# Performance work log

Hardware: AMD Instinct MI355X
Metric: run time of the kernel (lower is better)

The kernel has to match this reference:

```python
import jax, jax.numpy as jnp
import numpy as np

B, L, D = 2, 1024, 1024
H = 16
NL = 2
DFF = 4 * D
EPS = 1e-5
W_SCALE = 0.02


def rmsnorm(x, w):
    # x * rsqrt(mean(x^2, -1) + eps) * w   (computed in fp32 as in the torch code)
    xf = x.astype(jnp.float32)
    n = xf * jax.lax.rsqrt(jnp.mean(xf * xf, axis=-1, keepdims=True) + EPS)
    return n.astype(x.dtype) * w


def setup_inputs() -> dict:
    key = jax.random.key(0)
    ks = jax.random.split(key, 10)
    x = jax.random.normal(ks[0], (B, L, D), dtype=jnp.float32)
    # torch nn.Linear weight layout: [out_features, in_features]; y = x @ W.T + b
    qw = jax.random.normal(ks[1], (NL, D, D), dtype=jnp.float32) * W_SCALE
    kw = jax.random.normal(ks[2], (NL, D, D), dtype=jnp.float32) * W_SCALE
    vw = jax.random.normal(ks[3], (NL, D, D), dtype=jnp.float32) * W_SCALE
    ow = jax.random.normal(ks[4], (NL, D, D), dtype=jnp.float32) * W_SCALE
    pn_w = jnp.ones((NL, D), dtype=jnp.float32)
    ln_w = jnp.ones((NL, D), dtype=jnp.float32)
    fc_w = jax.random.normal(ks[5], (NL, DFF, D), dtype=jnp.float32) * W_SCALE
    fc2_w = jax.random.normal(ks[6], (NL, D, DFF), dtype=jnp.float32) * W_SCALE
    fc2_b = jnp.zeros((NL, D), dtype=jnp.float32)
    return {"x": x, "qw": qw, "kw": kw, "vw": vw, "ow": ow,
            "pn_w": pn_w, "ln_w": ln_w, "fc_w": fc_w, "fc2_w": fc2_w, "fc2_b": fc2_b}


def reference(x, qw, kw, vw, ow, pn_w, ln_w, fc_w, fc2_w, fc2_b):
    d = D // H
    for i in range(NL):
        # --- LinearAttention block (dropout=0 -> identity) ---
        h = rmsnorm(x, pn_w[i])                                   # [B,L,D]
        Q = (h @ qw[i].T).reshape(B, L, H, d)
        K = (h @ kw[i].T).reshape(B, L, H, d)
        V = (h @ vw[i].T).reshape(B, L, H, d)
        # outer-product state per position, cumulated over L (causal linear attn)
        W = jnp.einsum('blhd,blhe->blhde', K, V)                  # [B,L,H,d,d]
        W = jnp.cumsum(W, axis=1)
        a = jnp.einsum('blhd,blhde->blhe', Q, W).reshape(B, L, D)
        x = x + a @ ow[i].T
        # --- MLP block ---
        m = rmsnorm(x, ln_w[i])
        f = jax.nn.gelu(m @ fc_w[i].T, approximate=False)         # torch nn.GELU default = exact
        x = x + f @ fc2_w[i].T + fc2_b[i]
    return x
```

## Files before the change

kernel.cpp:

```cpp
#include <hip/hip_runtime.h>

#define BB 2
#define LL 1024
#define DD 1024
#define HH 16
#define HD 64
#define DFFN 4096
#define MM (BB*LL)
#define QS 3072

using u16 = unsigned short;
typedef __bf16 bf16x8 __attribute__((ext_vector_type(8)));
typedef float f32x4 __attribute__((ext_vector_type(4)));

__device__ __forceinline__ float b2f(u16 u) {
  union { unsigned int i; float f; } v; v.i = ((unsigned int)u) << 16; return v.f;
}
__device__ __forceinline__ u16 f2b(float f) {
  union { float f; unsigned int i; } v; v.f = f;
  unsigned int x = v.i;
  return (u16)((x + 0x7fffu + ((x >> 16) & 1u)) >> 16);
}
__device__ __forceinline__ float gelu_exact(float x) {
  return 0.5f * x * (1.0f + erff(x * 0.70710678118654752f));
}
__device__ __forceinline__ void gl2lds16(const void* g, void* l) {
  __builtin_amdgcn_global_load_lds((const __attribute__((address_space(1))) void*)g,
                                   (__attribute__((address_space(3))) void*)l, 16, 0, 0);
}

template<int N>
__device__ __forceinline__ void s_wait_vm() {
  if constexpr (N == 0)      asm volatile("s_waitcnt vmcnt(0) lgkmcnt(0)" ::: "memory");
  else if constexpr (N == 4) asm volatile("s_waitcnt vmcnt(4) lgkmcnt(0)" ::: "memory");
  else if constexpr (N == 6) asm volatile("s_waitcnt vmcnt(6) lgkmcnt(0)" ::: "memory");
  else if constexpr (N == 8) asm volatile("s_waitcnt vmcnt(8) lgkmcnt(0)" ::: "memory");
  __builtin_amdgcn_sched_barrier(0);
}

__global__ __launch_bounds__(256) void castw_kernel(const float* __restrict__ in,
                                                    u16* __restrict__ out, int n8) {
  int i = blockIdx.x * 256 + threadIdx.x;
  if (i >= n8) return;
  const float4 a = reinterpret_cast<const float4*>(in)[2 * i];
  const float4 b = reinterpret_cast<const float4*>(in)[2 * i + 1];
  uint4 o;
  o.x = (unsigned)f2b(a.x) | ((unsigned)f2b(a.y) << 16);
  o.y = (unsigned)f2b(a.z) | ((unsigned)f2b(a.w) << 16);
  o.z = (unsigned)f2b(b.x) | ((unsigned)f2b(b.y) << 16);
  o.w = (unsigned)f2b(b.z) | ((unsigned)f2b(b.w) << 16);
  reinterpret_cast<uint4*>(out)[i] = o;
}
__global__ __launch_bounds__(256) void castw3_kernel(const float* __restrict__ s0,
                                                     const float* __restrict__ s1,
                                                     const float* __restrict__ s2,
                                                     u16* __restrict__ out, int n8) {
  int i = blockIdx.x * 256 + threadIdx.x;
  if (i >= n8) return;
  const float* in = (blockIdx.y == 0) ? s0 : (blockIdx.y == 1) ? s1 : s2;
  u16* dst = out + (size_t)blockIdx.y * n8 * 8;
  const float4 a = reinterpret_cast<const float4*>(in)[2 * i];
  const float4 b = reinterpret_cast<const float4*>(in)[2 * i + 1];
  uint4 o;
  o.x = (unsigned)f2b(a.x) | ((unsigned)f2b(a.y) << 16);
  o.y = (unsigned)f2b(a.z) | ((unsigned)f2b(a.w) << 16);
  o.z = (unsigned)f2b(b.x) | ((unsigned)f2b(b.y) << 16);
  o.w = (unsigned)f2b(b.z) | ((unsigned)f2b(b.w) << 16);
  reinterpret_cast<uint4*>(dst)[i] = o;
}

__global__ __launch_bounds__(256) void init_out_kernel(float* __restrict__ out,
                                                       const float* __restrict__ resid,
                                                       const float* __restrict__ bias) {
  const int i = blockIdx.x * 256 + threadIdx.x;
  float4 v = reinterpret_cast<const float4*>(resid)[i];
  if (bias != nullptr) {
    const float4 bv = *reinterpret_cast<const float4*>(bias + ((i * 4) & (DD - 1)));
    v.x += bv.x; v.y += bv.y; v.z += bv.z; v.w += bv.w;
  }
  reinterpret_cast<float4*>(out)[i] = v;
}

__global__ __launch_bounds__(256) void rmsnorm_kernel(const float* __restrict__ x,
                                                      const float* __restrict__ w,
                                                      u16* __restrict__ out) {
  const int row = blockIdx.x, t = threadIdx.x;
  const float4 v = reinterpret_cast<const float4*>(x + (size_t)row * DD)[t];
  float ss = v.x*v.x + v.y*v.y + v.z*v.z + v.w*v.w;
  #pragma unroll
  for (int o = 32; o > 0; o >>= 1) ss += __shfl_down(ss, o);
  __shared__ float red[4];
  if ((t & 63) == 0) red[t >> 6] = ss;
  __syncthreads();
  const float inv = rsqrtf((red[0] + red[1] + red[2] + red[3]) * (1.0f / DD) + 1e-5f);
  const float4 wv = reinterpret_cast<const float4*>(w)[t];
  ushort4 o;
  o.x = f2b(v.x * inv * wv.x);
  o.y = f2b(v.y * inv * wv.y);
  o.z = f2b(v.z * inv * wv.z);
  o.w = f2b(v.w * inv * wv.w);
  reinterpret_cast<ushort4*>(out + (size_t)row * DD)[t] = o;
}

template<int ROWS, int NT>
__device__ __forceinline__ void dma32(const u16* __restrict__ g, int r0, int K, int kt,
                                      int t, u16* lds) {
  #pragma unroll
  for (int i = 0; i < ROWS * 4 / NT; i++) {
    const int c = i * NT + t;
    gl2lds16(g + (size_t)(r0 + (c >> 2)) * K + kt + (c & 3) * 8, &lds[c * 8]);
  }
}
__device__ __forceinline__ void mfma_tile32(const u16* Asb, const u16* Bsb,
                                            int wm, int wn, int fr, int fq, f32x4 acc[4][4]) {
  bf16x8 af[4], bfv[4];
  #pragma unroll
  for (int i = 0; i < 4; i++)
    af[i] = *reinterpret_cast<const bf16x8*>(&Asb[(wm + i * 16 + fr) * 32 + fq * 8]);
  #pragma unroll
  for (int j = 0; j < 4; j++)
    bfv[j] = *reinterpret_cast<const bf16x8*>(&Bsb[(wn + j * 16 + fr) * 32 + fq * 8]);
  #pragma unroll
  for (int i = 0; i < 4; i++)
    #pragma unroll
    for (int j = 0; j < 4; j++)
      acc[i][j] = __builtin_amdgcn_mfma_f32_16x16x32_bf16(af[i], bfv[j], acc[i][j], 0, 0, 0);
}

template<int BM, int BN>
__device__ __forceinline__ void gemm_pipeline(const u16* __restrict__ A,
                                              const u16* __restrict__ Wb,
                                              int K, int k0, int nt, int m0, int n0,
                                              u16* As, u16* Bs, int t,
                                              int wm, int wn, int fr, int fq,
                                              f32x4 acc[4][4]) {
  constexpr int NT = (BM / 64) * (BN / 64) * 64;
  constexpr int L = (BM + BN) * 4 / NT;
  dma32<BM, NT>(A, m0, K, k0, t, As);
  dma32<BN, NT>(Wb, n0, K, k0, t, Bs);
  dma32<BM, NT>(A, m0, K, k0 + 32, t, As + BM * 32);
  dma32<BN, NT>(Wb, n0, K, k0 + 32, t, Bs + BN * 32);
  int pb = 0;
  for (int tt = 0; tt < nt; ++tt) {
    if (tt + 1 < nt) s_wait_vm<L>(); else s_wait_vm<0>();
    __builtin_amdgcn_s_barrier();
    __builtin_amdgcn_sched_barrier(0);
    if (tt + 2 < nt) {
      int p2 = pb + 2; if (p2 >= 3) p2 -= 3;
      dma32<BM, NT>(A, m0, K, k0 + (tt + 2) * 32, t, As + p2 * BM * 32);
      dma32<BN, NT>(Wb, n0, K, k0 + (tt + 2) * 32, t, Bs + p2 * BN * 32);
      __builtin_amdgcn_sched_barrier(0);
    }
    mfma_tile32(As + pb * BM * 32, Bs + pb * BN * 32, wm, wn, fr, fq, acc);
    pb = (pb == 2) ? 0 : pb + 1;
  }
}

template<int BM, int BN, int ACT>
__global__ __launch_bounds__((BM/64)*(BN/64)*64)
void mfma_gemm(const u16* __restrict__ A, const u16* __restrict__ Wb,
               u16* __restrict__ Cb, int N, int K) {
  constexpr int WCOLS = BN / 64;
  __shared__ u16 As[3 * BM * 32];
  __shared__ u16 Bs[3 * BN * 32];
  const int t = threadIdx.x;
  const int lane = t & 63, w = t >> 6;
  const int wm = (w / WCOLS) * 64, wn = (w % WCOLS) * 64;
  const int m0 = blockIdx.y * BM, n0 = blockIdx.x * BN;
  const int fr = lane & 15, fq = lane >> 4;

  f32x4 acc[4][4] = {};
  gemm_pipeline<BM, BN>(A, Wb, K, 0, K / 32, m0, n0, As, Bs, t, wm, wn, fr, fq, acc);

  #pragma unroll
  for (int i = 0; i < 4; i++)
    #pragma unroll
    for (int j = 0; j < 4; j++)
      #pragma unroll
      for (int r = 0; r < 4; r++) {
        const int row = m0 + wm + i * 16 + fq * 4 + r;
        const int col = n0 + wn + j * 16 + fr;
        float val = acc[i][j][r];
        if (ACT == 1) val = gelu_exact(val);
        Cb[(size_t)row * N + col] = f2b(val);
      }
}

template<int BM, int BN, int SPLIT>
__global__ __launch_bounds__((BM/64)*(BN/64)*64)
void mfma_gemm_sk(const u16* __restrict__ A, const u16* __restrict__ Wb,
                  float* __restrict__ Co, int N, int K) {
  constexpr int WCOLS = BN / 64;
  __shared__ u16 As[3 * BM * 32];
  __shared__ u16 Bs[3 * BN * 32];
  const int t = threadIdx.x;
  const int lane = t & 63, w = t >> 6;
  const int wm = (w / WCOLS) * 64, wn = (w % WCOLS) * 64;
  const int m0 = blockIdx.y * BM, n0 = blockIdx.x * BN;
  const int fr = lane & 15, fq = lane >> 4;
  const int Kc = K / SPLIT, k0 = blockIdx.z * Kc;

  f32x4 acc[4][4] = {};
  gemm_pipeline<BM, BN>(A, Wb, K, k0, Kc / 32, m0, n0, As, Bs, t, wm, wn, fr, fq, acc);

  #pragma unroll
  for (int i = 0; i < 4; i++)
    #pragma unroll
    for (int j = 0; j < 4; j++)
      #pragma unroll
      for (int r = 0; r < 4; r++) {
        const int row = m0 + wm + i * 16 + fq * 4 + r;
        const int col = n0 + wn + j * 16 + fr;
        unsafeAtomicAdd(&Co[(size_t)row * N + col], acc[i][j][r]);
      }
}

__global__ __launch_bounds__(256) void kv_trans(const u16* __restrict__ QKV,
                                                u16* __restrict__ Kt, u16* __restrict__ Vt) {
  __shared__ u16 T[64][72];
  const int tile = blockIdx.x;
  const int h2 = blockIdx.y;
  const int b = blockIdx.z;
  const int h = h2 & 15, which = h2 >> 4;
  const int t = threadIdx.x;
  const int pos = t >> 2, d0 = (t & 3) * 16;
  const u16* src = QKV + ((size_t)(b * LL) + tile * 64 + pos) * QS + 1024 + which * 1024 + h * HD + d0;
  union { uint4 u[2]; u16 s[16]; } pk;
  pk.u[0] = reinterpret_cast<const uint4*>(src)[0];
  pk.u[1] = reinterpret_cast<const uint4*>(src)[1];
  #pragma unroll
  for (int j = 0; j < 16; j++) T[d0 + j][pos] = pk.s[j];
  __syncthreads();
  const int d = t >> 2, p0 = (t & 3) * 16;
  u16* dst = (which ? Vt : Kt) + ((size_t)(b * HH + h) * HD + d) * LL + tile * 64 + p0;
  union { uint4 u[2]; u16 s[16]; } ok;
  #pragma unroll
  for (int j = 0; j < 16; j++) ok.s[j] = T[d][p0 + j];
  reinterpret_cast<uint4*>(dst)[0] = ok.u[0];
  reinterpret_cast<uint4*>(dst)[1] = ok.u[1];
}

__global__ __launch_bounds__(256) void attn_phase1(const u16* __restrict__ QKV,
                                                   const u16* __restrict__ Kt,
                                                   const u16* __restrict__ Vt,
                                                   u16* __restrict__ Oa,
                                                   u16* __restrict__ Slt) {
  __shared__ u16 Ss[4][16][64];
  const int tile = blockIdx.x, h = blockIdx.y, b = blockIdx.z;
  const int t = threadIdx.x, lane = t & 63, w = t >> 6;
  const int fr = lane & 15, fq = lane >> 4;
  const size_t tok0 = (size_t)(b * LL + tile * 64);
  const size_t bh = (size_t)(b * HH + h);
  const u16* Qb  = QKV + tok0 * QS + h * HD;
  const u16* Kb  = Qb + 1024;
  const u16* Ktb = Kt + bh * (HD * LL) + tile * 64;
  const u16* Vtb = Vt + bh * (HD * LL) + tile * 64;

  bf16x8 aq[2], bk[4][2];
  #pragma unroll
  for (int kh = 0; kh < 2; kh++)
    aq[kh] = *reinterpret_cast<const bf16x8*>(Qb + (size_t)(16*w + fr) * QS + kh*32 + fq*8);
  #pragma unroll
  for (int n4 = 0; n4 < 4; n4++)
    #pragma unroll
    for (int kh = 0; kh < 2; kh++)
      bk[n4][kh] = *reinterpret_cast<const bf16x8*>(Kb + (size_t)(16*n4 + fr) * QS + kh*32 + fq*8);
  f32x4 sacc[4] = {};
  #pragma unroll
  for (int n4 = 0; n4 < 4; n4++) {
    sacc[n4] = __builtin_amdgcn_mfma_f32_16x16x32_bf16(aq[0], bk[n4][0], sacc[n4], 0, 0, 0);
    sacc[n4] = __builtin_amdgcn_mfma_f32_16x16x32_bf16(aq[1], bk[n4][1], sacc[n4], 0, 0, 0);
  }
  #pragma unroll
  for (int n4 = 0; n4 < 4; n4++)
    #pragma unroll
    for (int r = 0; r < 4; r++) {
      const bool keep = (16*w + 4*fq + r) >= (16*n4 + fr);
      Ss[w][4*fq + r][16*n4 + fr] = keep ? f2b(sacc[n4][r]) : (u16)0;
    }
  __syncthreads();

  bf16x8 va[2], kt[4][2];
  #pragma unroll
  for (int kh = 0; kh < 2; kh++)
    va[kh] = *reinterpret_cast<const bf16x8*>(Vtb + (size_t)(16*w + fr) * LL + kh*32 + fq*8);
  #pragma unroll
  for (int n4 = 0; n4 < 4; n4++)
    #pragma unroll
    for (int kh = 0; kh < 2; kh++)
      kt[n4][kh] = *reinterpret_cast<const bf16x8*>(Ktb + (size_t)(16*n4 + fr) * LL + kh*32 + fq*8);
  f32x4 lacc[4] = {};
  #pragma unroll
  for (int n4 = 0; n4 < 4; n4++) {
    lacc[n4] = __builtin_amdgcn_mfma_f32_16x16x32_bf16(va[0], kt[n4][0], lacc[n4], 0, 0, 0);
    lacc[n4] = __builtin_amdgcn_mfma_f32_16x16x32_bf16(va[1], kt[n4][1], lacc[n4], 0, 0, 0);
  }
  u16* So = Slt + (bh * 16 + tile) * 4096;
  #pragma unroll
  for (int n4 = 0; n4 < 4; n4++)
    #pragma unroll
    for (int r = 0; r < 4; r++)
      So[(size_t)(16*w + 4*fq + r) * 64 + 16*n4 + fr] = f2b(lacc[n4][r]);

  bf16x8 sa[2], vb[4][2];
  #pragma unroll
  for (int kh = 0; kh < 2; kh++)
    sa[kh] = *reinterpret_cast<const bf16x8*>(&Ss[w][fr][kh*32 + fq*8]);
  #pragma unroll
  for (int n4 = 0; n4 < 4; n4++)
    #pragma unroll
    for (int kh = 0; kh < 2; kh++)
      vb[n4][kh] = *reinterpret_cast<const bf16x8*>(Vtb + (size_t)(16*n4 + fr) * LL + kh*32 + fq*8);
  f32x4 oacc[4] = {};
  #pragma unroll
  for (int n4 = 0; n4 < 4; n4++) {
    oacc[n4] = __builtin_amdgcn_mfma_f32_16x16x32_bf16(sa[0], vb[n4][0], oacc[n4], 0, 0, 0);
    oacc[n4] = __builtin_amdgcn_mfma_f32_16x16x32_bf16(sa[1], vb[n4][1], oacc[n4], 0, 0, 0);
  }
  u16* Ob = Oa + (tok0 + 16*w) * DD + h * HD;
  #pragma unroll
  for (int n4 = 0; n4 < 4; n4++)
    #pragma unroll
    for (int r = 0; r < 4; r++)
      Ob[(size_t)(4*fq + r) * DD + 16*n4 + fr] = f2b(oacc[n4][r]);
}

__global__ __launch_bounds__(256) void attn_phase2(const u16* __restrict__ Slt,
                                                   u16* __restrict__ Wc) {
  const int rg = blockIdx.x, h = blockIdx.y, b = blockIdx.z;
  const size_t base = ((size_t)((b * HH + h) * 16)) * 4096 + rg * 512 + threadIdx.x * 2;
  float r0 = 0.f, r1 = 0.f;
  for (int tl = 0; tl < 16; tl++) {
    const size_t p = base + (size_t)tl * 4096;
    const unsigned d = *reinterpret_cast<const unsigned*>(Slt + p);
    *reinterpret_cast<unsigned*>(Wc + p) = (unsigned)f2b(r0) | ((unsigned)f2b(r1) << 16);
    r0 += b2f((u16)(d & 0xffff));
    r1 += b2f((u16)(d >> 16));
  }
}

__global__ __launch_bounds__(256) void attn_phase3(const u16* __restrict__ QKV,
                                                   const u16* __restrict__ Wc,
                                                   u16* __restrict__ Oa) {
  const int tile = blockIdx.x, h = blockIdx.y, b = blockIdx.z;
  const int t = threadIdx.x, lane = t & 63, w = t >> 6;
  const int fr = lane & 15, fq = lane >> 4;
  const size_t tok0 = (size_t)(b * LL + tile * 64);
  const size_t bh = (size_t)(b * HH + h);
  const u16* Qb = QKV + tok0 * QS + h * HD;
  const u16* Wb = Wc + (bh * 16 + tile) * 4096;

  bf16x8 aq[2], wb[4][2];
  #pragma unroll
  for (int kh = 0; kh < 2; kh++)
    aq[kh] = *reinterpret_cast<const bf16x8*>(Qb + (size_t)(16*w + fr) * QS + kh*32 + fq*8);
  #pragma unroll
  for (int n4 = 0; n4 < 4; n4++)
    #pragma unroll
    for (int kh = 0; kh < 2; kh++)
      wb[n4][kh] = *reinterpret_cast<const bf16x8*>(Wb + (size_t)(16*n4 + fr) * 64 + kh*32 + fq*8);
  f32x4 oacc[4] = {};
  #pragma unroll
  for (int n4 = 0; n4 < 4; n4++) {
    oacc[n4] = __builtin_amdgcn_mfma_f32_16x16x32_bf16(aq[0], wb[n4][0], oacc[n4], 0, 0, 0);
    oacc[n4] = __builtin_amdgcn_mfma_f32_16x16x32_bf16(aq[1], wb[n4][1], oacc[n4], 0, 0, 0);
  }
  u16* Ob = Oa + (tok0 + 16*w) * DD + h * HD;
  #pragma unroll
  for (int n4 = 0; n4 < 4; n4++)
    #pragma unroll
    for (int r = 0; r < 4; r++) {
      const size_t idx = (size_t)(4*fq + r) * DD + 16*n4 + fr;
      Ob[idx] = f2b(b2f(Ob[idx]) + oacc[n4][r]);
    }
}

extern "C" void kernel_launch(void* const* d_in, const int* in_sizes, int n_in,
                              void* d_out, int out_size, void* d_ws, size_t ws_size,
                              hipStream_t stream) {
  const float* x_in = (const float*)d_in[0];
  const float* qw   = (const float*)d_in[1];
  const float* kw   = (const float*)d_in[2];
  const float* vw   = (const float*)d_in[3];
  const float* ow   = (const float*)d_in[4];
  const float* pn   = (const float*)d_in[5];
  const float* ln   = (const float*)d_in[6];
  const float* fcw  = (const float*)d_in[7];
  const float* fc2w = (const float*)d_in[8];
  const float* fc2b = (const float*)d_in[9];

  char* ws = (char*)d_ws;
  u16* wbuf = (u16*)ws;
  u16* slt  = (u16*)ws;
  u16* wcum = (u16*)(ws + (size_t)(4 << 20));
  u16* h    = (u16*)(ws + (size_t)(8 << 20));
  u16* qkv  = (u16*)(ws + (size_t)(12 << 20));
  u16* f    = (u16*)(ws + (size_t)(12 << 20));
  u16* vt   = (u16*)(ws + (size_t)(24 << 20));
  u16* kt   = (u16*)(ws + (size_t)(28 << 20));
  float* xf = (float*)d_out;

  const int n8D = DD * DD / 8;
  const int n8F = DFFN * DD / 8;
  const int gInit = MM * DD / 4 / 256;

  for (int i = 0; i < 2; i++) {
    const float* qwi  = qw   + (size_t)i * DD * DD;
    const float* kwi  = kw   + (size_t)i * DD * DD;
    const float* vwi  = vw   + (size_t)i * DD * DD;
    const float* owi  = ow   + (size_t)i * DD * DD;
    const float* fcwi = fcw  + (size_t)i * DFFN * DD;
    const float* f2wi = fc2w + (size_t)i * DD * DFFN;
    const float* src  = (i == 0) ? x_in : xf;

    rmsnorm_kernel<<<MM, 256, 0, stream>>>(src, pn + i * DD, h);
    castw3_kernel<<<dim3(n8D / 256, 3), 256, 0, stream>>>(qwi, kwi, vwi, wbuf, n8D);
    mfma_gemm<128, 64, 0><<<dim3(QS / 64, MM / 128), 128, 0, stream>>>(
        h, wbuf, qkv, QS, DD);
    kv_trans<<<dim3(16, 32, BB), 256, 0, stream>>>(qkv, kt, vt);
    attn_phase1<<<dim3(16, HH, BB), 256, 0, stream>>>(qkv, kt, vt, h, slt);
    attn_phase2<<<dim3(8, HH, BB), 256, 0, stream>>>(slt, wcum);
    attn_phase3<<<dim3(16, HH, BB), 256, 0, stream>>>(qkv, wcum, h);
    castw_kernel<<<n8D / 256, 256, 0, stream>>>(owi, wbuf, n8D);
    init_out_kernel<<<gInit, 256, 0, stream>>>(xf, src, nullptr);
    mfma_gemm_sk<128, 64, 2><<<dim3(DD / 64, MM / 128, 2), 128, 0, stream>>>(
        h, wbuf, xf, DD, DD);
    rmsnorm_kernel<<<MM, 256, 0, stream>>>(xf, ln + i * DD, h);
    castw_kernel<<<n8F / 256, 256, 0, stream>>>(fcwi, wbuf, n8F);
    mfma_gemm<128, 64, 1><<<dim3(DFFN / 64, MM / 128), 128, 0, stream>>>(
        h, wbuf, f, DFFN, DD);
    castw_kernel<<<n8F / 256, 256, 0, stream>>>(f2wi, wbuf, n8F);
    float* co = (i == 1) ? (float*)d_out : xf;
    init_out_kernel<<<gInit, 256, 0, stream>>>(co, xf, fc2b + i * DD);
    mfma_gemm_sk<128, 64, 4><<<dim3(DD / 64, MM / 128, 4), 128, 0, stream>>>(
        f, wbuf, co, DD, DFFN);
  }
}
```

Before: 521.8 us.

## Deepen GEMM LDS pipeline to four stages and remap blocks across XCDs

The GEMM main loop goes from a 3-buffer ring prefetching two tiles ahead to a 4-buffer ring prefetching three ahead, with matching vmcnt waits. This hides more global-load latency. Both GEMM kernels also remap the linear block index so that consecutive tiles land on the same XCD, which should improve L2 reuse of A and W tiles. The cost is more LDS per block, which may lower occupancy, and the remap only applies when the block count is a multiple of 128.

```diff
diff --git a/kernel.cpp b/kernel.cpp
--- a/kernel.cpp
+++ b/kernel.cpp
@@ -31,11 +31,24 @@
 
 template<int N>
 __device__ __forceinline__ void s_wait_vm() {
-  if constexpr (N == 0)      asm volatile("s_waitcnt vmcnt(0) lgkmcnt(0)" ::: "memory");
-  else if constexpr (N == 4) asm volatile("s_waitcnt vmcnt(4) lgkmcnt(0)" ::: "memory");
-  else if constexpr (N == 6) asm volatile("s_waitcnt vmcnt(6) lgkmcnt(0)" ::: "memory");
-  else if constexpr (N == 8) asm volatile("s_waitcnt vmcnt(8) lgkmcnt(0)" ::: "memory");
+  if constexpr (N == 0)       asm volatile("s_waitcnt vmcnt(0) lgkmcnt(0)" ::: "memory");
+  else if constexpr (N == 4)  asm volatile("s_waitcnt vmcnt(4) lgkmcnt(0)" ::: "memory");
+  else if constexpr (N == 6)  asm volatile("s_waitcnt vmcnt(6) lgkmcnt(0)" ::: "memory");
+  else if constexpr (N == 8)  asm volatile("s_waitcnt vmcnt(8) lgkmcnt(0)" ::: "memory");
+  else if constexpr (N == 12) asm volatile("s_waitcnt vmcnt(12) lgkmcnt(0)" ::: "memory");
   __builtin_amdgcn_sched_barrier(0);
+}
+
+__device__ __forceinline__ void xcd_remap(int& bx, int& by, int& bz) {
+  const int gx = gridDim.x, gy = gridDim.y;
+  const int nb = gx * gy * gridDim.z;
+  int b = blockIdx.x + gx * (blockIdx.y + gy * blockIdx.z);
+  if ((nb & 127) == 0) {
+    const int xcd = b & 7, seq = b >> 3;
+    b = (((seq >> 4) << 3) + xcd) * 16 + (seq & 15);
+  }
+  bx = b % gx; const int rest = b / gx;
+  by = rest % gy; bz = rest / gy;
 }
 
 __global__ __launch_bounds__(256) void castw_kernel(const float* __restrict__ in,
@@ -136,23 +149,27 @@
                                               f32x4 acc[4][4]) {
   constexpr int NT = (BM / 64) * (BN / 64) * 64;
   constexpr int L = (BM + BN) * 4 / NT;
-  dma32<BM, NT>(A, m0, K, k0, t, As);
-  dma32<BN, NT>(Wb, n0, K, k0, t, Bs);
-  dma32<BM, NT>(A, m0, K, k0 + 32, t, As + BM * 32);
-  dma32<BN, NT>(Wb, n0, K, k0 + 32, t, Bs + BN * 32);
+  #pragma unroll
+  for (int s = 0; s < 3; ++s) {
+    dma32<BM, NT>(A, m0, K, k0 + s * 32, t, As + s * BM * 32);
+    dma32<BN, NT>(Wb, n0, K, k0 + s * 32, t, Bs + s * BN * 32);
+  }
   int pb = 0;
   for (int tt = 0; tt < nt; ++tt) {
-    if (tt + 1 < nt) s_wait_vm<L>(); else s_wait_vm<0>();
+    const int ahead = nt - 1 - tt;
+    if (ahead >= 2)      s_wait_vm<2 * L>();
+    else if (ahead == 1) s_wait_vm<L>();
+    else                 s_wait_vm<0>();
     __builtin_amdgcn_s_barrier();
     __builtin_amdgcn_sched_barrier(0);
-    if (tt + 2 < nt) {
-      int p2 = pb + 2; if (p2 >= 3) p2 -= 3;
-      dma32<BM, NT>(A, m0, K, k0 + (tt + 2) * 32, t, As + p2 * BM * 32);
-      dma32<BN, NT>(Wb, n0, K, k0 + (tt + 2) * 32, t, Bs + p2 * BN * 32);
+    if (tt + 3 < nt) {
+      int p3 = pb + 3; if (p3 >= 4) p3 -= 4;
+      dma32<BM, NT>(A, m0, K, k0 + (tt + 3) * 32, t, As + p3 * BM * 32);
+      dma32<BN, NT>(Wb, n0, K, k0 + (tt + 3) * 32, t, Bs + p3 * BN * 32);
       __builtin_amdgcn_sched_barrier(0);
     }
     mfma_tile32(As + pb * BM * 32, Bs + pb * BN * 32, wm, wn, fr, fq, acc);
-    pb = (pb == 2) ? 0 : pb + 1;
+    pb = (pb + 1) & 3;
   }
 }
 
@@ -161,12 +178,14 @@
 void mfma_gemm(const u16* __restrict__ A, const u16* __restrict__ Wb,
                u16* __restrict__ Cb, int N, int K) {
   constexpr int WCOLS = BN / 64;
-  __shared__ u16 As[3 * BM * 32];
-  __shared__ u16 Bs[3 * BN * 32];
+  __shared__ u16 As[4 * BM * 32];
+  __shared__ u16 Bs[4 * BN * 32];
+  int bx, by, bz;
+  xcd_remap(bx, by, bz);
   const int t = threadIdx.x;
   const int lane = t & 63, w = t >> 6;
   const int wm = (w / WCOLS) * 64, wn = (w % WCOLS) * 64;
-  const int m0 = blockIdx.y * BM, n0 = blockIdx.x * BN;
+  const int m0 = by * BM, n0 = bx * BN;
   const int fr = lane & 15, fq = lane >> 4;
 
   f32x4 acc[4][4] = {};
@@ -191,14 +210,16 @@
 void mfma_gemm_sk(const u16* __restrict__ A, const u16* __restrict__ Wb,
                   float* __restrict__ Co, int N, int K) {
   constexpr int WCOLS = BN / 64;
-  __shared__ u16 As[3 * BM * 32];
-  __shared__ u16 Bs[3 * BN * 32];
+  __shared__ u16 As[4 * BM * 32];
+  __shared__ u16 Bs[4 * BN * 32];
+  int bx, by, bz;
+  xcd_remap(bx, by, bz);
   const int t = threadIdx.x;
   const int lane = t & 63, w = t >> 6;
   const int wm = (w / WCOLS) * 64, wn = (w % WCOLS) * 64;
-  const int m0 = blockIdx.y * BM, n0 = blockIdx.x * BN;
+  const int m0 = by * BM, n0 = bx * BN;
   const int fr = lane & 15, fq = lane >> 4;
-  const int Kc = K / SPLIT, k0 = blockIdx.z * Kc;
+  const int Kc = K / SPLIT, k0 = bz * Kc;
 
   f32x4 acc[4][4] = {};
   gemm_pipeline<BM, BN>(A, Wb, K, k0, Kc / 32, m0, n0, As, Bs, t, wm, wn, fr, fq, acc);
```

Result: slower. 583.5 us (+11.8%).
